# Kernel optimization log

Hardware: AMD Instinct MI355X
Metric: run time of the kernel (lower is better)

The kernel has to match this reference:

```python
import jax, jax.numpy as jnp
import numpy as np

A, B, D = 64, 128, 256   # batch, route nodes, feature_dim
H, C = 64, 32            # hidden_capsule, center_num
NUM_ITERS = 3


def _squash(t, axis=-1):
    sq = jnp.sum(t * t, axis=axis, keepdims=True)
    return (sq / (1.0 + sq)) * t / jnp.sqrt(sq)


def _route(priors, n_iters):
    # priors: [K, A, R, D]; dynamic routing over axis=2 (R).
    # Original keeps logits of priors' full shape, but they stay constant
    # along D (init zeros, delta has keepdim on last axis), so [K,A,R,1]
    # is exactly equivalent and avoids a redundant [K,A,R,D] buffer.
    logits = jnp.zeros(priors.shape[:-1] + (1,), priors.dtype)
    outputs = None
    for i in range(n_iters):
        probs = jax.nn.softmax(logits, axis=2)          # [K,A,R,1]
        outputs = _squash(jnp.sum(probs * priors, axis=2, keepdims=True))  # [K,A,1,D]
        if i != n_iters - 1:
            logits = logits + jnp.sum(priors * outputs, axis=-1, keepdims=True)
    return outputs


def setup_inputs() -> dict:
    key = jax.random.key(0)
    k1, k2, k3 = jax.random.split(key, 3)
    x = jax.random.normal(k1, (A, B, D), dtype=jnp.float32)
    route_weights1 = jax.random.normal(k2, (H, D, D), dtype=jnp.float32)
    route_weights = jax.random.normal(k3, (C, D, D), dtype=jnp.float32)
    return {"x": x, "route_weights1": route_weights1, "route_weights": route_weights}


def reference(x, route_weights1, route_weights):
    # stage 1: priors1[h,a,b,:] = x[a,b,:] @ W1[h]  -> [H,A,B,D]
    priors1 = jnp.einsum('abd,hde->habe', x, route_weights1)
    out1 = _route(priors1, NUM_ITERS)                  # [H,A,1,D]
    out1 = jnp.transpose(out1[:, :, 0, :], (1, 0, 2))  # squeeze + transpose(0,1) -> [A,H,D]
    # stage 2: priors[c,a,h,:] = out1[a,h,:] @ W[c]   -> [C,A,H,D]
    priors = jnp.einsum('ahd,cde->cahe', out1, route_weights)
    out = _route(priors, NUM_ITERS)                    # [C,A,1,D]
    return out[:, :, 0, :]                             # squeeze -> [C,A,D]
```

## Files before the change

kernel.cpp:

```cpp
#include <hip/hip_runtime.h>
#include <hip/hip_bf16.h>

typedef __attribute__((ext_vector_type(8))) short bf16x8;
typedef __attribute__((ext_vector_type(4))) float f32x4;
typedef unsigned short u16;
typedef unsigned int u32;

__device__ __forceinline__ u32 bf16_rne(float f) {
  u32 u = __float_as_uint(f);
  return (u + 0x7FFFu + ((u >> 16) & 1u)) >> 16;
}
__device__ __forceinline__ float bf16_val(u32 b) { return __uint_as_float(b << 16); }

__device__ __forceinline__ void g2l16(const u16* g, u16* l) {
  __builtin_amdgcn_global_load_lds(
      (const __attribute__((address_space(1))) u32*)g,
      (__attribute__((address_space(3))) u32*)l, 16, 0, 0);
}

__global__ void split_arr(const float* __restrict__ in,
                          u16* __restrict__ hi, u16* __restrict__ lo, int n4) {
  int i = blockIdx.x * 256 + threadIdx.x;
  if (i >= n4) return;
  float4 v = ((const float4*)in)[i];
  u32 h0 = bf16_rne(v.x), h1 = bf16_rne(v.y), h2 = bf16_rne(v.z), h3 = bf16_rne(v.w);
  u32 l0 = bf16_rne(v.x - bf16_val(h0));
  u32 l1 = bf16_rne(v.y - bf16_val(h1));
  u32 l2 = bf16_rne(v.z - bf16_val(h2));
  u32 l3 = bf16_rne(v.w - bf16_val(h3));
  ushort4 hv; hv.x = (u16)h0; hv.y = (u16)h1; hv.z = (u16)h2; hv.w = (u16)h3;
  ushort4 lv; lv.x = (u16)l0; lv.y = (u16)l1; lv.z = (u16)l2; lv.w = (u16)l3;
  ((ushort4*)hi)[i] = hv;
  ((ushort4*)lo)[i] = lv;
}

__global__ void split_transpose256(const float* __restrict__ in,
                                   u16* __restrict__ hi, u16* __restrict__ lo) {
  __shared__ float tile[32][33];
  const size_t off = (size_t)blockIdx.z * 65536;
  const int tx = threadIdx.x, ty = threadIdx.y;
#pragma unroll
  for (int i = 0; i < 4; ++i) {
    int y = blockIdx.y * 32 + ty + i * 8;
    int x = blockIdx.x * 32 + tx;
    tile[ty + i * 8][tx] = in[off + (size_t)y * 256 + x];
  }
  __syncthreads();
#pragma unroll
  for (int i = 0; i < 4; ++i) {
    float v = tile[tx][ty + i * 8];
    u32 hb = bf16_rne(v);
    u32 lb = bf16_rne(v - bf16_val(hb));
    size_t idx = off + (size_t)(blockIdx.x * 32 + ty + i * 8) * 256 + blockIdx.y * 32 + tx;
    hi[idx] = (u16)hb;
    lo[idx] = (u16)lb;
  }
}

template <int R>
__global__ __launch_bounds__(512, 2) void caps_route(
    const u16* __restrict__ Ahi_g,
    const u16* __restrict__ Alo_g,
    const u16* __restrict__ Whi,
    const u16* __restrict__ Wlo,
    u16* __restrict__ o1hi, u16* __restrict__ o1lo,
    float* __restrict__ outp,
    int KN, int stage) {
  constexpr int APB = 256 / R;
  constexpr int SEG = APB / 2;
  constexpr int MTS = 8 / SEG;
  constexpr int ABS = (R == 128) ? 5 : 4;
  __shared__ u16 BUF[2][32768];
  __shared__ __align__(16) float wlog[4][256];
  __shared__ __align__(16) float probs[256];
  __shared__ float sqpart[4][4];

  const int tid = threadIdx.x;
  const int w = tid >> 6, lane = tid & 63, q = lane >> 4, li = lane & 15;
  const int mg = w >> 2, eg = w & 3;
  const int kk = blockIdx.x >> ABS;
  const int ab = blockIdx.x & ((1 << ABS) - 1);

  const int sub = lane >> 2, p = lane & 3;
  const int gslot = p ^ ((sub >> 1) & 3);
  const size_t goff = (size_t)w * 4096 + sub * 256 + gslot * 8;
  const u16* gAh = Ahi_g + (size_t)ab * 65536 + goff;
  const u16* gAl = Alo_g + (size_t)ab * 65536 + goff;
  const u16* gWh = Whi  + (size_t)kk * 65536 + goff;
  const u16* gWl = Wlo  + (size_t)kk * 65536 + goff;
  u16* l0 = &BUF[0][0] + w * 512 + lane * 8;
  u16* l1 = &BUF[1][0] + w * 512 + lane * 8;

#define STAGE8(ko, l)                          \
  do {                                         \
    g2l16(gAh + (ko), (l));                    \
    g2l16(gAh + (ko) + 32768, (l) + 4096);     \
    g2l16(gAl + (ko), (l) + 8192);             \
    g2l16(gAl + (ko) + 32768, (l) + 12288);    \
    g2l16(gWh + (ko), (l) + 16384);            \
    g2l16(gWh + (ko) + 32768, (l) + 20480);    \
    g2l16(gWl + (ko), (l) + 24576);            \
    g2l16(gWl + (ko) + 32768, (l) + 28672);    \
  } while (0)

  const int rslot = q ^ ((li >> 1) & 3);
  const int fbase = li * 32 + rslot * 8;

  f32x4 acc[8][4] = {};

  STAGE8(0, l0);

#pragma unroll
  for (int ks = 0; ks < 8; ++ks) {
    const u16* B0 = (ks & 1) ? &BUF[1][0] : &BUF[0][0];
    if (ks < 7) {
      const int ko = (ks + 1) * 32;
      if (ks & 1) STAGE8(ko, l0); else STAGE8(ko, l1);
      asm volatile("s_waitcnt vmcnt(8)" ::: "memory");
    } else {
      asm volatile("s_waitcnt vmcnt(0)" ::: "memory");
    }
    __builtin_amdgcn_s_barrier();
    asm volatile("" ::: "memory");
    bf16x8 bh[4], bl[4];
#pragma unroll
    for (int ct = 0; ct < 4; ++ct) {
      const u16* bp = B0 + 16384 + (eg * 4 + ct) * 512 + fbase;
      bh[ct] = *(const bf16x8*)bp;
      bl[ct] = *(const bf16x8*)(bp + 8192);
    }
    const u16* aB = B0 + mg * 4096 + fbase;
    bf16x8 ahc = *(const bf16x8*)(aB);
    bf16x8 alc = *(const bf16x8*)(aB + 8192);
#pragma unroll
    for (int mt = 0; mt < 8; ++mt) {
      bf16x8 ahn, aln;
      if (mt < 7) {
        ahn = *(const bf16x8*)(aB + (mt + 1) * 512);
        aln = *(const bf16x8*)(aB + (mt + 1) * 512 + 8192);
      }
      __builtin_amdgcn_s_setprio(1);
#pragma unroll
      for (int ct = 0; ct < 4; ++ct)
        acc[mt][ct] = __builtin_amdgcn_mfma_f32_16x16x32_bf16(alc, bh[ct], acc[mt][ct], 0, 0, 0);
#pragma unroll
      for (int ct = 0; ct < 4; ++ct)
        acc[mt][ct] = __builtin_amdgcn_mfma_f32_16x16x32_bf16(ahc, bl[ct], acc[mt][ct], 0, 0, 0);
#pragma unroll
      for (int ct = 0; ct < 4; ++ct)
        acc[mt][ct] = __builtin_amdgcn_mfma_f32_16x16x32_bf16(ahc, bh[ct], acc[mt][ct], 0, 0, 0);
      __builtin_amdgcn_s_setprio(0);
      if (mt < 7) { ahc = ahn; alc = aln; }
    }
    asm volatile("" ::: "memory");
    __builtin_amdgcn_s_barrier();
  }
#undef STAGE8

  const float invR = 1.0f / R;
  const int rb = mg * 128;
  float v[SEG][4];
  float lg0 = 0.f, lg1 = 0.f;

  for (int iter = 0; iter < 3; ++iter) {
    float4 p4[8];
    if (iter == 0) {
#pragma unroll
      for (int mt = 0; mt < 8; ++mt) {
        p4[mt].x = invR; p4[mt].y = invR; p4[mt].z = invR; p4[mt].w = invR;
      }
    } else {
#pragma unroll
      for (int mt = 0; mt < 8; ++mt)
        p4[mt] = *(const float4*)&probs[rb + mt * 16 + q * 4];
    }
    float s[SEG][4];
#pragma unroll
    for (int sg = 0; sg < SEG; ++sg) {
#pragma unroll
      for (int ct = 0; ct < 4; ++ct) {
        float t = 0.f;
#pragma unroll
        for (int mi = 0; mi < MTS; ++mi) {
          const int mt = sg * MTS + mi;
          t += p4[mt].x * acc[mt][ct][0] + p4[mt].y * acc[mt][ct][1] +
               p4[mt].z * acc[mt][ct][2] + p4[mt].w * acc[mt][ct][3];
        }
        t += __shfl_xor(t, 16);
        t += __shfl_xor(t, 32);
        s[sg][ct] = t;
      }
    }
#pragma unroll
    for (int sg = 0; sg < SEG; ++sg) {
      float ss = s[sg][0] * s[sg][0] + s[sg][1] * s[sg][1] +
                 s[sg][2] * s[sg][2] + s[sg][3] * s[sg][3];
      ss += __shfl_xor(ss, 1); ss += __shfl_xor(ss, 2);
      ss += __shfl_xor(ss, 4); ss += __shfl_xor(ss, 8);
      if (lane == 0) sqpart[mg * SEG + sg][eg] = ss;
    }
    __syncthreads();
#pragma unroll
    for (int sg = 0; sg < SEG; ++sg) {
      const int a = mg * SEG + sg;
      float sq = sqpart[a][0] + sqpart[a][1] + sqpart[a][2] + sqpart[a][3];
      float scale = (sq > 0.f) ? sq / ((1.0f + sq) * sqrtf(sq)) : 0.f;
#pragma unroll
      for (int ct = 0; ct < 4; ++ct) v[sg][ct] = s[sg][ct] * scale;
    }

    if (iter < 2) {
#pragma unroll
      for (int mt = 0; mt < 8; ++mt) {
        const int sg = mt / MTS;
        float tt[4];
#pragma unroll
        for (int rr = 0; rr < 4; ++rr) {
          float t = acc[mt][0][rr] * v[sg][0] + acc[mt][1][rr] * v[sg][1] +
                    acc[mt][2][rr] * v[sg][2] + acc[mt][3][rr] * v[sg][3];
          t += __shfl_xor(t, 1); t += __shfl_xor(t, 2);
          t += __shfl_xor(t, 4); t += __shfl_xor(t, 8);
          tt[rr] = t;
        }
        if (li == 0)
          *(float4*)&wlog[eg][rb + mt * 16 + q * 4] =
              make_float4(tt[0], tt[1], tt[2], tt[3]);
      }
      __syncthreads();
      if (R == 128) {
        int r0 = rb + lane, r1 = r0 + 64;
        lg0 += wlog[0][r0] + wlog[1][r0] + wlog[2][r0] + wlog[3][r0];
        lg1 += wlog[0][r1] + wlog[1][r1] + wlog[2][r1] + wlog[3][r1];
        float m = fmaxf(lg0, lg1);
#pragma unroll
        for (int d2 = 1; d2 < 64; d2 <<= 1) m = fmaxf(m, __shfl_xor(m, d2));
        float e0 = __expf(lg0 - m), e1 = __expf(lg1 - m);
        float zz = e0 + e1;
#pragma unroll
        for (int d2 = 1; d2 < 64; d2 <<= 1) zz += __shfl_xor(zz, d2);
        float inv = 1.0f / zz;
        probs[r0] = e0 * inv;
        probs[r1] = e1 * inv;
      } else {
        int r0 = rb + lane, r1 = r0 + 64;
        lg0 += wlog[0][r0] + wlog[1][r0] + wlog[2][r0] + wlog[3][r0];
        lg1 += wlog[0][r1] + wlog[1][r1] + wlog[2][r1] + wlog[3][r1];
        float m0 = lg0, m1 = lg1;
#pragma unroll
        for (int d2 = 1; d2 < 64; d2 <<= 1) {
          m0 = fmaxf(m0, __shfl_xor(m0, d2));
          m1 = fmaxf(m1, __shfl_xor(m1, d2));
        }
        float e0 = __expf(lg0 - m0), e1 = __expf(lg1 - m1);
        float z0 = e0, z1 = e1;
#pragma unroll
        for (int d2 = 1; d2 < 64; d2 <<= 1) {
          z0 += __shfl_xor(z0, d2);
          z1 += __shfl_xor(z1, d2);
        }
        probs[r0] = e0 / z0;
        probs[r1] = e1 / z1;
      }
      asm volatile("s_waitcnt lgkmcnt(0)" ::: "memory");
    }
  }

  if (q == 0) {
#pragma unroll
    for (int sg = 0; sg < SEG; ++sg) {
      const int ag = ab * APB + mg * SEG + sg;
      if (stage == 1) {
        size_t ob = ((size_t)ag * KN + kk) * 256;
#pragma unroll
        for (int ct = 0; ct < 4; ++ct) {
          int e = eg * 64 + ct * 16 + li;
          u32 hb = bf16_rne(v[sg][ct]);
          u32 lb = bf16_rne(v[sg][ct] - bf16_val(hb));
          o1hi[ob + e] = (u16)hb;
          o1lo[ob + e] = (u16)lb;
        }
      } else {
        size_t ob = ((size_t)kk * 64 + ag) * 256;
#pragma unroll
        for (int ct = 0; ct < 4; ++ct) {
          int e = eg * 64 + ct * 16 + li;
          outp[ob + e] = v[sg][ct];
        }
      }
    }
  }
}

extern "C" void kernel_launch(void* const* d_in, const int* in_sizes, int n_in,
                              void* d_out, int out_size, void* d_ws, size_t ws_size,
                              hipStream_t stream) {
  const float* x  = (const float*)d_in[0];
  const float* w1 = (const float*)d_in[1];
  const float* wc = (const float*)d_in[2];
  float* out = (float*)d_out;

  char* ws = (char*)d_ws;
  u16* w1hi = (u16*)(ws);
  u16* w1lo = (u16*)(ws + (8u << 20));
  u16* wchi = (u16*)(ws + (16u << 20));
  u16* wclo = (u16*)(ws + (20u << 20));
  u16* xhi  = (u16*)(ws + (24u << 20));
  u16* xlo  = (u16*)(ws + (28u << 20));
  u16* o1hi = (u16*)(ws + (32u << 20));
  u16* o1lo = (u16*)(ws + (34u << 20));

  split_arr<<<2048, 256, 0, stream>>>(x, xhi, xlo, 524288);
  split_transpose256<<<dim3(8, 8, 64), dim3(32, 8), 0, stream>>>(w1, w1hi, w1lo);
  split_transpose256<<<dim3(8, 8, 32), dim3(32, 8), 0, stream>>>(wc, wchi, wclo);
  caps_route<128><<<64 * 32, 512, 0, stream>>>(xhi, xlo, w1hi, w1lo, o1hi, o1lo, nullptr, 64, 1);
  caps_route<64><<<32 * 16, 512, 0, stream>>>(o1hi, o1lo, wchi, wclo, nullptr, nullptr, out, 32, 2);
}
```

Baseline: 373.7 us.

## Halve caps_route block tile to 128 rows and reassign load roles per wave

The routing kernel now uses 256-thread blocks, each covering one 128-row group instead of two, so twice as many blocks are launched and each block needs much less LDS. Loading is split by wave role: two waves stream the W hi/lo slices into a single buffer, and two waves stream A hi/lo into a double buffer. The next stage is issued right after the W fragments are pulled into registers. The A-fragment register prefetch and the setprio hints are dropped. The aim is more concurrent blocks and better latency hiding, at the cost of each W tile being fetched twice as often from global memory and cache.

```diff
diff --git a/kernel.cpp b/kernel.cpp
--- a/kernel.cpp
+++ b/kernel.cpp
@@ -58,7 +58,7 @@
 }
 
 template <int R>
-__global__ __launch_bounds__(512, 2) void caps_route(
+__global__ __launch_bounds__(256, 2) void caps_route(
     const u16* __restrict__ Ahi_g,
     const u16* __restrict__ Alo_g,
     const u16* __restrict__ Whi,
@@ -66,99 +66,81 @@
     u16* __restrict__ o1hi, u16* __restrict__ o1lo,
     float* __restrict__ outp,
     int KN, int stage) {
-  constexpr int APB = 256 / R;
-  constexpr int SEG = APB / 2;
+  constexpr int APB = 128 / R;
+  constexpr int SEG = APB;
   constexpr int MTS = 8 / SEG;
-  constexpr int ABS = (R == 128) ? 5 : 4;
-  __shared__ u16 BUF[2][32768];
-  __shared__ __align__(16) float wlog[4][256];
-  __shared__ __align__(16) float probs[256];
-  __shared__ float sqpart[4][4];
+  constexpr int ABS = (R == 128) ? 6 : 5;
+  __shared__ __align__(16) u16 Ab[2][8192];
+  __shared__ __align__(16) u16 Wb[16384];
+  __shared__ __align__(16) float wlog[4][128];
+  __shared__ __align__(16) float probs[128];
+  __shared__ float sqpart[2][4];
 
   const int tid = threadIdx.x;
   const int w = tid >> 6, lane = tid & 63, q = lane >> 4, li = lane & 15;
-  const int mg = w >> 2, eg = w & 3;
+  const int eg = w;
   const int kk = blockIdx.x >> ABS;
   const int ab = blockIdx.x & ((1 << ABS) - 1);
 
   const int sub = lane >> 2, p = lane & 3;
   const int gslot = p ^ ((sub >> 1) & 3);
-  const size_t goff = (size_t)w * 4096 + sub * 256 + gslot * 8;
-  const u16* gAh = Ahi_g + (size_t)ab * 65536 + goff;
-  const u16* gAl = Alo_g + (size_t)ab * 65536 + goff;
-  const u16* gWh = Whi  + (size_t)kk * 65536 + goff;
-  const u16* gWl = Wlo  + (size_t)kk * 65536 + goff;
-  u16* l0 = &BUF[0][0] + w * 512 + lane * 8;
-  u16* l1 = &BUF[1][0] + w * 512 + lane * 8;
-
-#define STAGE8(ko, l)                          \
-  do {                                         \
-    g2l16(gAh + (ko), (l));                    \
-    g2l16(gAh + (ko) + 32768, (l) + 4096);     \
-    g2l16(gAl + (ko), (l) + 8192);             \
-    g2l16(gAl + (ko) + 32768, (l) + 12288);    \
-    g2l16(gWh + (ko), (l) + 16384);            \
-    g2l16(gWh + (ko) + 32768, (l) + 20480);    \
-    g2l16(gWl + (ko), (l) + 24576);            \
-    g2l16(gWl + (ko) + 32768, (l) + 28672);    \
-  } while (0)
+  const size_t lane_off = (size_t)sub * 256 + gslot * 8;
+  const u16* gsrc;
+  u16* ldst;
+  if (w == 0)      { gsrc = Whi   + (size_t)kk * 65536 + lane_off; ldst = &Wb[0]       + lane * 8; }
+  else if (w == 1) { gsrc = Wlo   + (size_t)kk * 65536 + lane_off; ldst = &Wb[8192]    + lane * 8; }
+  else if (w == 2) { gsrc = Ahi_g + (size_t)ab * 32768 + lane_off; ldst = &Ab[0][0]    + lane * 8; }
+  else             { gsrc = Alo_g + (size_t)ab * 32768 + lane_off; ldst = &Ab[0][4096] + lane * 8; }
+
+  auto STAGE = [&](int ko, int nb) {
+    if (w < 2) {
+#pragma unroll
+      for (int i = 0; i < 16; ++i) g2l16(gsrc + ko + i * 4096, ldst + i * 512);
+    } else {
+      u16* d = ldst + nb * 8192;
+#pragma unroll
+      for (int i = 0; i < 8; ++i) g2l16(gsrc + ko + i * 4096, d + i * 512);
+    }
+  };
 
   const int rslot = q ^ ((li >> 1) & 3);
   const int fbase = li * 32 + rslot * 8;
 
   f32x4 acc[8][4] = {};
 
-  STAGE8(0, l0);
+  STAGE(0, 0);
+  asm volatile("s_waitcnt vmcnt(0)" ::: "memory");
+  __builtin_amdgcn_s_barrier();
 
 #pragma unroll
   for (int ks = 0; ks < 8; ++ks) {
-    const u16* B0 = (ks & 1) ? &BUF[1][0] : &BUF[0][0];
-    if (ks < 7) {
-      const int ko = (ks + 1) * 32;
-      if (ks & 1) STAGE8(ko, l0); else STAGE8(ko, l1);
-      asm volatile("s_waitcnt vmcnt(8)" ::: "memory");
-    } else {
-      asm volatile("s_waitcnt vmcnt(0)" ::: "memory");
-    }
-    __builtin_amdgcn_s_barrier();
-    asm volatile("" ::: "memory");
     bf16x8 bh[4], bl[4];
 #pragma unroll
     for (int ct = 0; ct < 4; ++ct) {
-      const u16* bp = B0 + 16384 + (eg * 4 + ct) * 512 + fbase;
+      const u16* bp = &Wb[(eg * 4 + ct) * 512] + fbase;
       bh[ct] = *(const bf16x8*)bp;
       bl[ct] = *(const bf16x8*)(bp + 8192);
     }
-    const u16* aB = B0 + mg * 4096 + fbase;
-    bf16x8 ahc = *(const bf16x8*)(aB);
-    bf16x8 alc = *(const bf16x8*)(aB + 8192);
+    asm volatile("s_waitcnt lgkmcnt(0)" ::: "memory");
+    __builtin_amdgcn_s_barrier();
+    if (ks < 7) STAGE((ks + 1) * 32, (ks + 1) & 1);
+    const u16* aB = &Ab[ks & 1][0] + fbase;
 #pragma unroll
     for (int mt = 0; mt < 8; ++mt) {
-      bf16x8 ahn, aln;
-      if (mt < 7) {
-        ahn = *(const bf16x8*)(aB + (mt + 1) * 512);
-        aln = *(const bf16x8*)(aB + (mt + 1) * 512 + 8192);
-      }
-      __builtin_amdgcn_s_setprio(1);
-#pragma unroll
-      for (int ct = 0; ct < 4; ++ct)
-        acc[mt][ct] = __builtin_amdgcn_mfma_f32_16x16x32_bf16(alc, bh[ct], acc[mt][ct], 0, 0, 0);
-#pragma unroll
-      for (int ct = 0; ct < 4; ++ct)
-        acc[mt][ct] = __builtin_amdgcn_mfma_f32_16x16x32_bf16(ahc, bl[ct], acc[mt][ct], 0, 0, 0);
-#pragma unroll
-      for (int ct = 0; ct < 4; ++ct)
-        acc[mt][ct] = __builtin_amdgcn_mfma_f32_16x16x32_bf16(ahc, bh[ct], acc[mt][ct], 0, 0, 0);
-      __builtin_amdgcn_s_setprio(0);
-      if (mt < 7) { ahc = ahn; alc = aln; }
-    }
-    asm volatile("" ::: "memory");
+      bf16x8 ah = *(const bf16x8*)(aB + mt * 512);
+      bf16x8 al = *(const bf16x8*)(aB + mt * 512 + 4096);
+#pragma unroll
+      for (int ct = 0; ct < 4; ++ct) {
+        acc[mt][ct] = __builtin_amdgcn_mfma_f32_16x16x32_bf16(al, bh[ct], acc[mt][ct], 0, 0, 0);
+        acc[mt][ct] = __builtin_amdgcn_mfma_f32_16x16x32_bf16(ah, bl[ct], acc[mt][ct], 0, 0, 0);
+        acc[mt][ct] = __builtin_amdgcn_mfma_f32_16x16x32_bf16(ah, bh[ct], acc[mt][ct], 0, 0, 0);
+      }
+    }
+    asm volatile("s_waitcnt vmcnt(0)" ::: "memory");
     __builtin_amdgcn_s_barrier();
   }
-#undef STAGE8
 
   const float invR = 1.0f / R;
-  const int rb = mg * 128;
   float v[SEG][4];
   float lg0 = 0.f, lg1 = 0.f;
 
@@ -172,7 +154,7 @@
     } else {
 #pragma unroll
       for (int mt = 0; mt < 8; ++mt)
-        p4[mt] = *(const float4*)&probs[rb + mt * 16 + q * 4];
+        p4[mt] = *(const float4*)&probs[mt * 16 + q * 4];
     }
     float s[SEG][4];
 #pragma unroll
@@ -197,13 +179,12 @@
                  s[sg][2] * s[sg][2] + s[sg][3] * s[sg][3];
       ss += __shfl_xor(ss, 1); ss += __shfl_xor(ss, 2);
       ss += __shfl_xor(ss, 4); ss += __shfl_xor(ss, 8);
-      if (lane == 0) sqpart[mg * SEG + sg][eg] = ss;
+      if (lane == 0) sqpart[sg][eg] = ss;
     }
     __syncthreads();
 #pragma unroll
     for (int sg = 0; sg < SEG; ++sg) {
-      const int a = mg * SEG + sg;
-      float sq = sqpart[a][0] + sqpart[a][1] + sqpart[a][2] + sqpart[a][3];
+      float sq = sqpart[sg][0] + sqpart[sg][1] + sqpart[sg][2] + sqpart[sg][3];
       float scale = (sq > 0.f) ? sq / ((1.0f + sq) * sqrtf(sq)) : 0.f;
 #pragma unroll
       for (int ct = 0; ct < 4; ++ct) v[sg][ct] = s[sg][ct] * scale;
@@ -223,12 +204,11 @@
           tt[rr] = t;
         }
         if (li == 0)
-          *(float4*)&wlog[eg][rb + mt * 16 + q * 4] =
-              make_float4(tt[0], tt[1], tt[2], tt[3]);
+          *(float4*)&wlog[eg][mt * 16 + q * 4] = make_float4(tt[0], tt[1], tt[2], tt[3]);
       }
       __syncthreads();
       if (R == 128) {
-        int r0 = rb + lane, r1 = r0 + 64;
+        int r0 = lane, r1 = lane + 64;
         lg0 += wlog[0][r0] + wlog[1][r0] + wlog[2][r0] + wlog[3][r0];
         lg1 += wlog[0][r1] + wlog[1][r1] + wlog[2][r1] + wlog[3][r1];
         float m = fmaxf(lg0, lg1);
@@ -242,7 +222,7 @@
         probs[r0] = e0 * inv;
         probs[r1] = e1 * inv;
       } else {
-        int r0 = rb + lane, r1 = r0 + 64;
+        int r0 = lane, r1 = lane + 64;
         lg0 += wlog[0][r0] + wlog[1][r0] + wlog[2][r0] + wlog[3][r0];
         lg1 += wlog[0][r1] + wlog[1][r1] + wlog[2][r1] + wlog[3][r1];
         float m0 = lg0, m1 = lg1;
@@ -268,7 +248,7 @@
   if (q == 0) {
 #pragma unroll
     for (int sg = 0; sg < SEG; ++sg) {
-      const int ag = ab * APB + mg * SEG + sg;
+      const int ag = ab * APB + sg;
       if (stage == 1) {
         size_t ob = ((size_t)ag * KN + kk) * 256;
 #pragma unroll
@@ -312,6 +292,6 @@
   split_arr<<<2048, 256, 0, stream>>>(x, xhi, xlo, 524288);
   split_transpose256<<<dim3(8, 8, 64), dim3(32, 8), 0, stream>>>(w1, w1hi, w1lo);
   split_transpose256<<<dim3(8, 8, 32), dim3(32, 8), 0, stream>>>(wc, wchi, wclo);
-  caps_route<128><<<64 * 32, 512, 0, stream>>>(xhi, xlo, w1hi, w1lo, o1hi, o1lo, nullptr, 64, 1);
-  caps_route<64><<<32 * 16, 512, 0, stream>>>(o1hi, o1lo, wchi, wclo, nullptr, nullptr, out, 32, 2);
-}
+  caps_route<128><<<64 * 64, 256, 0, stream>>>(xhi, xlo, w1hi, w1lo, o1hi, o1lo, nullptr, 64, 1);
+  caps_route<64><<<32 * 32, 256, 0, stream>>>(o1hi, o1lo, wchi, wclo, nullptr, nullptr, out, 32, 2);
+}
```

Measured after the change: 357.2 us. 4.4% less time.
